# Performance work log

Hardware: AMD Instinct MI355X
Metric: run time of the kernel (lower is better)

## Reference

```python
import jax, jax.numpy as jnp
import numpy as np

N_NODES = 100000
N_EDGES = 1600000
NEG_SLOPE = 0.2  # PyG GATConv default


def _glorot(key, shape):
    fan = sum(shape[:2]) if len(shape) > 1 else shape[0] * 2
    s = jnp.sqrt(6.0 / fan)
    return jax.random.uniform(key, shape, jnp.float32, -s, s)


def gat_layer(x, src, dst, edge_attr, W, a_src, a_dst, We, a_e, b, heads, out_ch, concat):
    """Faithful PyG GATConv (add_self_loops=True, fill_value='mean', edge_dim set)."""
    n = x.shape[0]
    # self-loop edge_attr = mean of incoming edge_attr per dst node (0 if none)
    deg = jax.ops.segment_sum(jnp.ones((src.shape[0],), edge_attr.dtype), dst, num_segments=n)
    loop_attr = jax.ops.segment_sum(edge_attr, dst, num_segments=n) / jnp.maximum(deg, 1.0)[:, None]
    loop = jnp.arange(n, dtype=src.dtype)
    src_f = jnp.concatenate([src, loop])
    dst_f = jnp.concatenate([dst, loop])
    ea = jnp.concatenate([edge_attr, loop_attr], axis=0)
    # node transform -> [n, H, C]
    h = (x @ W).reshape(n, heads, out_ch)
    al_src = jnp.sum(h * a_src, axis=-1)  # [n, H]
    al_dst = jnp.sum(h * a_dst, axis=-1)  # [n, H]
    e = (ea @ We).reshape(-1, heads, out_ch)
    al_e = jnp.sum(e * a_e, axis=-1)      # [Ef, H]
    alpha = jax.nn.leaky_relu(al_src[src_f] + al_dst[dst_f] + al_e, negative_slope=NEG_SLOPE)
    # segment softmax over destination nodes (every node has a self loop)
    m = jax.ops.segment_max(alpha, dst_f, num_segments=n)
    ex = jnp.exp(alpha - m[dst_f])
    den = jax.ops.segment_sum(ex, dst_f, num_segments=n)
    att = ex / den[dst_f]                 # [Ef, H]
    out = jax.ops.segment_sum(att[:, :, None] * h[src_f], dst_f, num_segments=n)  # [n, H, C]
    out = out.reshape(n, heads * out_ch) if concat else out.mean(axis=1)
    return out + b


def setup_inputs() -> dict:
    key = jax.random.key(0)
    ks = jax.random.split(key, 20)
    x = jax.random.normal(ks[0], (N_NODES, 5), jnp.float32)
    edge_index = jax.random.randint(ks[1], (2, N_EDGES), 0, N_NODES, jnp.int64)
    edge_attr = jax.random.normal(ks[2], (N_EDGES, 2), jnp.float32)
    # conv1: in=5, out=32, heads=4, concat -> 128
    p = {
        "W1": _glorot(ks[3], (5, 128)), "aS1": _glorot(ks[4], (4, 32)),
        "aD1": _glorot(ks[5], (4, 32)), "We1": _glorot(ks[6], (2, 128)),
        "aE1": _glorot(ks[7], (4, 32)), "b1": jnp.zeros((128,), jnp.float32),
        # conv2: in=128, out=32, heads=2, concat -> 64
        "W2": _glorot(ks[8], (128, 64)), "aS2": _glorot(ks[9], (2, 32)),
        "aD2": _glorot(ks[10], (2, 32)), "We2": _glorot(ks[11], (2, 64)),
        "aE2": _glorot(ks[12], (2, 32)), "b2": jnp.zeros((64,), jnp.float32),
        # conv3: in=64, out=1, heads=1, concat=False
        "W3": _glorot(ks[13], (64, 1)), "aS3": _glorot(ks[14], (1, 1)),
        "aD3": _glorot(ks[15], (1, 1)), "We3": _glorot(ks[16], (2, 1)),
        "aE3": _glorot(ks[17], (1, 1)), "b3": jnp.zeros((1,), jnp.float32),
    }
    return {"x": x, "edge_index": edge_index, "edge_attr": edge_attr, **p}


def reference(x, edge_index, edge_attr,
              W1, aS1, aD1, We1, aE1, b1,
              W2, aS2, aD2, We2, aE2, b2,
              W3, aS3, aD3, We3, aE3, b3):
    src, dst = edge_index[0], edge_index[1]
    h = gat_layer(x, src, dst, edge_attr, W1, aS1, aD1, We1, aE1, b1, 4, 32, True)
    h = jax.nn.elu(h)  # dropout is identity in eval
    h = gat_layer(h, src, dst, edge_attr, W2, aS2, aD2, We2, aE2, b2, 2, 32, True)
    h = jax.nn.elu(h)
    h = gat_layer(h, src, dst, edge_attr, W3, aS3, aD3, We3, aE3, b3, 1, 1, False)
    return jax.nn.sigmoid(h).squeeze(-1)  # [N]
```

## Files before the change

### kernel.cpp

```cpp
#include <hip/hip_runtime.h>
#include <math.h>

#define NN 100000
#define NE 1600000
#define NPB 256
#define NPB_SHIFT 8
#define NB ((NN + NPB - 1) / NPB)
#define NCHUNK 512
#define CH ((NE + NCHUNK - 1) / NCHUNK)
#define LOG2E 1.44269504088896f

typedef __attribute__((ext_vector_type(8))) short short8v;
typedef __attribute__((ext_vector_type(4))) float f32x4;

__device__ __forceinline__ float lrelu(float x) { return fmaxf(x, 0.2f * x); }
__device__ __forceinline__ float elu1(float x) { return x > 0.f ? x : (__expf(x) - 1.f); }
__device__ __forceinline__ float fexp2(float x) {
#if __has_builtin(__builtin_amdgcn_exp2f)
    return __builtin_amdgcn_exp2f(x);
#else
    return exp2f(x);
#endif
}
__device__ __forceinline__ unsigned bf16rne(float f) {
    unsigned u = __float_as_uint(f);
    return (u + 0x7FFFu + ((u >> 16) & 1u)) >> 16;
}
__device__ __forceinline__ float bf16lo(unsigned u) { return __uint_as_float(u << 16); }
__device__ __forceinline__ float bf16hi(unsigned u) {
    return __uint_as_float(u & 0xFFFF0000u);
}
__device__ __forceinline__ void split2(float x0, float x1, unsigned& hp, unsigned& lp) {
    unsigned h0 = bf16rne(x0), h1 = bf16rne(x1);
    float r0 = x0 - __uint_as_float(h0 << 16);
    float r1 = x1 - __uint_as_float(h1 << 16);
    hp = h0 | (h1 << 16);
    lp = bf16rne(r0) | (bf16rne(r1) << 16);
}

__global__ void __launch_bounds__(256) k_binA0(const int* __restrict__ dst,
                                               int* __restrict__ bucket_cnt) {
    __shared__ int hist[NB];
    int t = threadIdx.x;
    for (int b = t; b < NB; b += 256) hist[b] = 0;
    __syncthreads();
    int c0 = blockIdx.x * CH, c1 = min(NE, c0 + CH);
    for (int e = c0 + t; e < c1; e += 256) atomicAdd(&hist[dst[e] >> NPB_SHIFT], 1);
    __syncthreads();
    for (int b = t; b < NB; b += 256)
        if (hist[b]) atomicAdd(&bucket_cnt[b], hist[b]);
}

__global__ void __launch_bounds__(512) k_bscan(const int* __restrict__ bucket_cnt,
                                               int* __restrict__ bucket_base,
                                               int* __restrict__ bucket_tail) {
    __shared__ int s[512];
    int t = threadIdx.x;
    int v = (t < NB) ? bucket_cnt[t] : 0;
    s[t] = v;
    __syncthreads();
    for (int off = 1; off < 512; off <<= 1) {
        int x = (t >= off) ? s[t - off] : 0;
        __syncthreads();
        if (t >= off) s[t] += x;
        __syncthreads();
    }
    if (t < NB) {
        int ex = s[t] - v;
        bucket_base[t] = ex;
        bucket_tail[t] = ex;
        if (t == NB - 1) bucket_base[NB] = s[t];
    }
}

__global__ void __launch_bounds__(256) k_binA2(const int* __restrict__ src,
                                               const int* __restrict__ dst,
                                               const float* __restrict__ ea,
                                               int* __restrict__ bucket_tail,
                                               uint2* __restrict__ binned,
                                               unsigned char* __restrict__ dstb) {
    __shared__ int hist[NB], pre[NB], cursor[NB], base_l[NB];
    __shared__ int psum[256];
    __shared__ uint2 lrec[CH];
    __shared__ int lds_d[CH];
    int t = threadIdx.x;
    for (int b = t; b < NB; b += 256) hist[b] = 0;
    __syncthreads();
    int c0 = blockIdx.x * CH, c1 = min(NE, c0 + CH);
    int cnt = c1 - c0;
    for (int i = t; i < cnt; i += 256) atomicAdd(&hist[dst[c0 + i] >> NPB_SHIFT], 1);
    __syncthreads();
    int b0 = t << 1, b1 = b0 + 1;
    int h0 = (b0 < NB) ? hist[b0] : 0;
    int h1 = (b1 < NB) ? hist[b1] : 0;
    psum[t] = h0 + h1;
    __syncthreads();
    for (int off = 1; off < 256; off <<= 1) {
        int x = (t >= off) ? psum[t - off] : 0;
        __syncthreads();
        if (t >= off) psum[t] += x;
        __syncthreads();
    }
    int ex = psum[t] - (h0 + h1);
    if (b0 < NB) { pre[b0] = ex;      cursor[b0] = ex; }
    if (b1 < NB) { pre[b1] = ex + h0; cursor[b1] = ex + h0; }
    for (int b = t; b < NB; b += 256) {
        int h = hist[b];
        if (h) base_l[b] = atomicAdd(&bucket_tail[b], h);
    }
    __syncthreads();
    for (int i = t; i < cnt; i += 256) {
        int e = c0 + i;
        int d = dst[e];
        int bkt = d >> NPB_SHIFT;
        int lpos = atomicAdd(&cursor[bkt], 1);
        unsigned pk = bf16rne(ea[2 * e]) | (bf16rne(ea[2 * e + 1]) << 16);
        lrec[lpos] = make_uint2((unsigned)src[e], pk);
        lds_d[lpos] = d;
    }
    __syncthreads();
    for (int i = t; i < cnt; i += 256) {
        int d = lds_d[i];
        int bkt = d >> NPB_SHIFT;
        int gpos = base_l[bkt] + (i - pre[bkt]);
        binned[gpos] = lrec[i];
        dstb[gpos] = (unsigned char)(d & (NPB - 1));
    }
}

__global__ void __launch_bounds__(256) k_binB(const int* __restrict__ bucket_base,
                                              const uint2* __restrict__ binned,
                                              const unsigned char* __restrict__ dstb,
                                              int* __restrict__ rowptr,
                                              uint2* __restrict__ edges,
                                              float* __restrict__ la) {
    __shared__ int hist[NPB], pre[NPB], cursor[NPB];
    __shared__ float ea0s[NPB], ea1s[NPB];
    int b = blockIdx.x, t = threadIdx.x;
    int bb = bucket_base[b], be = bucket_base[b + 1];
    int nb0 = b << NPB_SHIFT;
    hist[t] = 0;
    ea0s[t] = 0.f;
    ea1s[t] = 0.f;
    __syncthreads();
    for (int e = bb + t; e < be; e += 256) atomicAdd(&hist[dstb[e]], 1);
    __syncthreads();
    int v = hist[t];
    pre[t] = v;
    __syncthreads();
    for (int off = 1; off < 256; off <<= 1) {
        int x = (t >= off) ? pre[t - off] : 0;
        __syncthreads();
        if (t >= off) pre[t] += x;
        __syncthreads();
    }
    int ex = pre[t] - v;
    if (nb0 + t <= NN) rowptr[nb0 + t] = bb + ex;
    cursor[t] = bb + ex;
    __syncthreads();
    for (int e = bb + t; e < be; e += 256) {
        uint2 rec = binned[e];
        unsigned char d = dstb[e];
        int pos = atomicAdd(&cursor[d], 1);
        edges[pos] = rec;
        atomicAdd(&ea0s[d], bf16lo(rec.y));
        atomicAdd(&ea1s[d], bf16hi(rec.y));
    }
    __syncthreads();
    int n = nb0 + t;
    if (n < NN) {
        float dg = fmaxf((float)v, 1.0f);
        la[2 * n] = ea0s[t] / dg;
        la[2 * n + 1] = ea1s[t] / dg;
    }
}

__global__ void k_const(const float* __restrict__ We1, const float* __restrict__ aE1,
                        const float* __restrict__ We2, const float* __restrict__ aE2,
                        const float* __restrict__ We3, const float* __restrict__ aE3,
                        const float* __restrict__ W1, const float* __restrict__ aS1,
                        const float* __restrict__ aD1, float* __restrict__ cbuf) {
    int t = threadIdx.x;
    if (t < 8) {
        int d = t >> 2, hd = t & 3;
        float s = 0.f;
        for (int c = 0; c < 32; c++) s += We1[d * 128 + hd * 32 + c] * aE1[hd * 32 + c];
        cbuf[t] = s * LOG2E;
    } else if (t < 12) {
        int idx = t - 8, d = idx >> 1, hd = idx & 1;
        float s = 0.f;
        for (int c = 0; c < 32; c++) s += We2[d * 64 + hd * 32 + c] * aE2[hd * 32 + c];
        cbuf[t] = s * LOG2E;
    } else if (t < 14) {
        cbuf[t] = We3[t - 12] * aE3[0] * LOG2E;
    } else if (t >= 16 && t < 56) {
        int r = (t - 16) % 20, hd = r / 5, i = r % 5;
        const float* a = (t - 16 < 20) ? aS1 : aD1;
        float s = 0.f;
        for (int c = 0; c < 32; c++) s += W1[i * 128 + hd * 32 + c] * a[hd * 32 + c];
        cbuf[t] = s * LOG2E;
    }
}

__global__ void k_w2t(const float* __restrict__ W2, unsigned short* __restrict__ W2th,
                      unsigned short* __restrict__ W2tl) {
    int i = blockIdx.x * 256 + threadIdx.x;
    if (i >= 64 * 128) return;
    int c = i >> 7, k = i & 127;
    float v = W2[k * 64 + c];
    unsigned h = bf16rne(v);
    float hf = __uint_as_float(h << 16);
    unsigned lo = bf16rne(v - hf);
    W2th[c * 128 + k] = (unsigned short)h;
    W2tl[c * 128 + k] = (unsigned short)lo;
}

__global__ void k_prep1(const float* __restrict__ x, const float* __restrict__ vsd,
                        float4* __restrict__ xp, float4* __restrict__ als1,
                        float4* __restrict__ ald1) {
    int n = blockIdx.x * blockDim.x + threadIdx.x;
    if (n >= NN) return;
    float x0 = x[5 * n], x1 = x[5 * n + 1], x2 = x[5 * n + 2], x3 = x[5 * n + 3],
          x4 = x[5 * n + 4];
    xp[2 * n] = make_float4(x0, x1, x2, x3);
    xp[2 * n + 1] = make_float4(x4, 0.f, 0.f, 0.f);
    float sv[4], dv[4];
#pragma unroll
    for (int hd = 0; hd < 4; hd++) {
        const float* vS = vsd + hd * 5;
        const float* vD = vsd + 20 + hd * 5;
        sv[hd] = x0 * vS[0] + x1 * vS[1] + x2 * vS[2] + x3 * vS[3] + x4 * vS[4];
        dv[hd] = x0 * vD[0] + x1 * vD[1] + x2 * vD[2] + x3 * vD[3] + x4 * vD[4];
    }
    als1[n] = make_float4(sv[0], sv[1], sv[2], sv[3]);
    ald1[n] = make_float4(dv[0], dv[1], dv[2], dv[3]);
}

__global__ void k_agg1(const int* __restrict__ rowptr, const uint2* __restrict__ edges,
                       const float4* __restrict__ xp, const float* __restrict__ als1,
                       const float* __restrict__ ald1, const float* __restrict__ la,
                       const float* __restrict__ me, float* __restrict__ xw) {
    int t = blockIdx.x * blockDim.x + threadIdx.x;
    if (t >= NN * 4) return;
    int n = t >> 2, hd = t & 3;
    float me0 = me[hd], me1 = me[4 + hd];
    float aldn = ald1[t];
    float aself = lrelu(als1[t] + aldn + la[2 * n] * me0 + la[2 * n + 1] * me1);
    int start = rowptr[n], end = rowptr[n + 1];
    float den = 1.f;
    float4 xa = xp[2 * n];
    float xb = xp[2 * n + 1].x;
    float a0 = xa.x, a1 = xa.y, a2 = xa.z, a3 = xa.w, a4 = xb;
    int e = start;
    if ((e & 1) && e < end) {
        uint2 ep = edges[e];
        int s = (int)ep.x;
        float a = lrelu(als1[s * 4 + hd] + aldn + bf16lo(ep.y) * me0 + bf16hi(ep.y) * me1);
        float p = fexp2(a - aself);
        den += p;
        float4 sa = xp[2 * s];
        float sb = xp[2 * s + 1].x;
        a0 += p * sa.x; a1 += p * sa.y; a2 += p * sa.z; a3 += p * sa.w; a4 += p * sb;
        e++;
    }
    for (; e + 1 < end; e += 2) {
        uint4 two = *(const uint4*)(edges + e);
        int s0 = (int)two.x, s1 = (int)two.z;
        unsigned pk0 = two.y, pk1 = two.w;
        float l0 = als1[s0 * 4 + hd];
        float l1 = als1[s1 * 4 + hd];
        float4 sa0 = xp[2 * s0];
        float sb0 = xp[2 * s0 + 1].x;
        float4 sa1 = xp[2 * s1];
        float sb1 = xp[2 * s1 + 1].x;
        float av0 = lrelu(l0 + aldn + bf16lo(pk0) * me0 + bf16hi(pk0) * me1);
        float av1 = lrelu(l1 + aldn + bf16lo(pk1) * me0 + bf16hi(pk1) * me1);
        float p0 = fexp2(av0 - aself);
        float p1 = fexp2(av1 - aself);
        den += p0 + p1;
        a0 += p0 * sa0.x + p1 * sa1.x;
        a1 += p0 * sa0.y + p1 * sa1.y;
        a2 += p0 * sa0.z + p1 * sa1.z;
        a3 += p0 * sa0.w + p1 * sa1.w;
        a4 += p0 * sb0 + p1 * sb1;
    }
    if (e < end) {
        uint2 ep = edges[e];
        int s = (int)ep.x;
        float a = lrelu(als1[s * 4 + hd] + aldn + bf16lo(ep.y) * me0 + bf16hi(ep.y) * me1);
        float p = fexp2(a - aself);
        den += p;
        float4 sa = xp[2 * s];
        float sb = xp[2 * s + 1].x;
        a0 += p * sa.x; a1 += p * sa.y; a2 += p * sa.z; a3 += p * sa.w; a4 += p * sb;
    }
    float r = 1.f / den;
    float* w = xw + (size_t)n * 20 + hd * 5;
    w[0] = a0 * r;
    w[1] = a1 * r;
    w[2] = a2 * r;
    w[3] = a3 * r;
    w[4] = a4 * r;
}

__global__ void __launch_bounds__(128) k_l2trans(
        const float* __restrict__ xw, const float* __restrict__ W1,
        const float* __restrict__ b1, const unsigned short* __restrict__ W2th,
        const unsigned short* __restrict__ W2tl,
        const float* __restrict__ aS2, const float* __restrict__ aD2,
        unsigned short* __restrict__ h2q, float* __restrict__ als2,
        float* __restrict__ ald2) {
    __shared__ float wstage[32 * 20];
    __shared__ unsigned short Ahi[4096];
    __shared__ unsigned short Alo[4096];
    int nb = blockIdx.x * 32, t = threadIdx.x;
    {
        int base = nb * 20;
        for (int idx = t; idx < 32 * 20; idx += 128) wstage[idx] = xw[base + idx];
    }
    __syncthreads();
    {
        int nl = t >> 2, g = t & 3;
        int w = nl >> 4, row = nl & 15;
#pragma unroll
        for (int kt = 0; kt < 4; ++kt) {
            int ch0 = kt * 32 + g * 8;
            float4 va = *(const float4*)(b1 + ch0);
            float4 vb = *(const float4*)(b1 + ch0 + 4);
            const float* wp = wstage + nl * 20 + kt * 5;
#pragma unroll
            for (int i = 0; i < 5; ++i) {
                float wi = wp[i];
                float4 A = *(const float4*)(W1 + i * 128 + ch0);
                float4 B = *(const float4*)(W1 + i * 128 + ch0 + 4);
                va.x += wi * A.x; va.y += wi * A.y; va.z += wi * A.z; va.w += wi * A.w;
                vb.x += wi * B.x; vb.y += wi * B.y; vb.z += wi * B.z; vb.w += wi * B.w;
            }
            unsigned hp0, hp1, hp2, hp3, lp0, lp1, lp2, lp3;
            split2(elu1(va.x), elu1(va.y), hp0, lp0);
            split2(elu1(va.z), elu1(va.w), hp1, lp1);
            split2(elu1(vb.x), elu1(vb.y), hp2, lp2);
            split2(elu1(vb.z), elu1(vb.w), hp3, lp3);
            int cidx = (((w * 4 + kt) * 64) + g * 16 + row) * 8;
            *(uint4*)(Ahi + cidx) = make_uint4(hp0, hp1, hp2, hp3);
            *(uint4*)(Alo + cidx) = make_uint4(lp0, lp1, lp2, lp3);
        }
    }
    int l = t & 63, w = t >> 6;
    int g = l >> 4, row16 = l & 15;
    f32x4 acc0 = {0.f, 0.f, 0.f, 0.f}, acc1 = acc0, acc2 = acc0, acc3 = acc0;
    int w4 = w * 4;
#pragma unroll
    for (int kt = 0; kt < 4; ++kt) {
        int abase = ((w4 + kt) * 64 + l) * 8;
        short8v ah = *(const short8v*)(Ahi + abase);
        short8v al = *(const short8v*)(Alo + abase);
        int kb = kt * 32 + g * 8;
        {
            short8v bh = *(const short8v*)(W2th + row16 * 128 + kb);
            short8v bl = *(const short8v*)(W2tl + row16 * 128 + kb);
            acc0 = __builtin_amdgcn_mfma_f32_16x16x32_bf16(ah, bh, acc0, 0, 0, 0);
            acc0 = __builtin_amdgcn_mfma_f32_16x16x32_bf16(al, bh, acc0, 0, 0, 0);
            acc0 = __builtin_amdgcn_mfma_f32_16x16x32_bf16(ah, bl, acc0, 0, 0, 0);
        }
        {
            short8v bh = *(const short8v*)(W2th + (16 + row16) * 128 + kb);
            short8v bl = *(const short8v*)(W2tl + (16 + row16) * 128 + kb);
            acc1 = __builtin_amdgcn_mfma_f32_16x16x32_bf16(ah, bh, acc1, 0, 0, 0);
            acc1 = __builtin_amdgcn_mfma_f32_16x16x32_bf16(al, bh, acc1, 0, 0, 0);
            acc1 = __builtin_amdgcn_mfma_f32_16x16x32_bf16(ah, bl, acc1, 0, 0, 0);
        }
        {
            short8v bh = *(const short8v*)(W2th + (32 + row16) * 128 + kb);
            short8v bl = *(const short8v*)(W2tl + (32 + row16) * 128 + kb);
            acc2 = __builtin_amdgcn_mfma_f32_16x16x32_bf16(ah, bh, acc2, 0, 0, 0);
            acc2 = __builtin_amdgcn_mfma_f32_16x16x32_bf16(al, bh, acc2, 0, 0, 0);
            acc2 = __builtin_amdgcn_mfma_f32_16x16x32_bf16(ah, bl, acc2, 0, 0, 0);
        }
        {
            short8v bh = *(const short8v*)(W2th + (48 + row16) * 128 + kb);
            short8v bl = *(const short8v*)(W2tl + (48 + row16) * 128 + kb);
            acc3 = __builtin_amdgcn_mfma_f32_16x16x32_bf16(ah, bh, acc3, 0, 0, 0);
            acc3 = __builtin_amdgcn_mfma_f32_16x16x32_bf16(al, bh, acc3, 0, 0, 0);
            acc3 = __builtin_amdgcn_mfma_f32_16x16x32_bf16(ah, bl, acc3, 0, 0, 0);
        }
    }
    {
        int nodeb = nb + w * 16 + g * 4;
#pragma unroll
        for (int nt = 0; nt < 4; ++nt) {
            f32x4 A = (nt == 0) ? acc0 : (nt == 1) ? acc1 : (nt == 2) ? acc2 : acc3;
#pragma unroll
            for (int r = 0; r < 4; ++r) {
                float v = A[r];
                float u = __shfl_xor(v, 1);
                if (!(l & 1)) {
                    unsigned pk = bf16rne(v) | (bf16rne(u) << 16);
                    int node = nodeb + r;
                    int ch = nt * 16 + row16;
                    *(unsigned*)(h2q + (size_t)node * 64 + ch) = pk;
                }
            }
        }
        float aSv0 = aS2[row16], aSv1 = aS2[16 + row16];
        float aSv2 = aS2[32 + row16], aSv3 = aS2[48 + row16];
        float aDv0 = aD2[row16], aDv1 = aD2[16 + row16];
        float aDv2 = aD2[32 + row16], aDv3 = aD2[48 + row16];
#pragma unroll
        for (int r = 0; r < 4; ++r) {
            float pS0 = acc0[r] * aSv0 + acc1[r] * aSv1;
            float pS1 = acc2[r] * aSv2 + acc3[r] * aSv3;
            float pD0 = acc0[r] * aDv0 + acc1[r] * aDv1;
            float pD1 = acc2[r] * aDv2 + acc3[r] * aDv3;
#pragma unroll
            for (int off = 1; off < 16; off <<= 1) {
                pS0 += __shfl_xor(pS0, off);
                pS1 += __shfl_xor(pS1, off);
                pD0 += __shfl_xor(pD0, off);
                pD1 += __shfl_xor(pD1, off);
            }
            if (row16 == 0) {
                int node = nodeb + r;
                als2[node * 2 + 0] = pS0 * LOG2E;
                als2[node * 2 + 1] = pS1 * LOG2E;
                ald2[node * 2 + 0] = pD0 * LOG2E;
                ald2[node * 2 + 1] = pD1 * LOG2E;
            }
        }
    }
}

__global__ void k_agg2(const int* __restrict__ rowptr, const uint2* __restrict__ edges,
                       const unsigned short* __restrict__ h2q,
                       const float* __restrict__ als2, const float* __restrict__ ald2,
                       const float* __restrict__ la, const float* __restrict__ me,
                       const float* __restrict__ b2, const float* __restrict__ W3,
                       float* __restrict__ h3) {
    int t = blockIdx.x * blockDim.x + threadIdx.x;
    if (t >= NN * 4) return;
    int n = t >> 2, sub = t & 3, hd = sub >> 1, qh = sub & 1;
    int cbase = hd * 32 + qh * 16;
    float me0 = me[hd], me1 = me[2 + hd];
    float aldn = ald2[n * 2 + hd];
    float aself = lrelu(als2[n * 2 + hd] + aldn + la[2 * n] * me0 + la[2 * n + 1] * me1);
    int start = rowptr[n], end = rowptr[n + 1];
    float den = 1.f;
    float acc[16];
    {
        const uint4* hp = (const uint4*)(h2q + (size_t)n * 64 + cbase);
        uint4 u0 = hp[0], u1 = hp[1];
        acc[0] = bf16lo(u0.x); acc[1] = bf16hi(u0.x);
        acc[2] = bf16lo(u0.y); acc[3] = bf16hi(u0.y);
        acc[4] = bf16lo(u0.z); acc[5] = bf16hi(u0.z);
        acc[6] = bf16lo(u0.w); acc[7] = bf16hi(u0.w);
        acc[8] = bf16lo(u1.x); acc[9] = bf16hi(u1.x);
        acc[10] = bf16lo(u1.y); acc[11] = bf16hi(u1.y);
        acc[12] = bf16lo(u1.z); acc[13] = bf16hi(u1.z);
        acc[14] = bf16lo(u1.w); acc[15] = bf16hi(u1.w);
    }
    int e = start;
    if ((e & 1) && e < end) {
        uint2 ep = edges[e];
        int s = (int)ep.x;
        float a = lrelu(als2[s * 2 + hd] + aldn + bf16lo(ep.y) * me0 + bf16hi(ep.y) * me1);
        float p = fexp2(a - aself);
        den += p;
        const uint4* sp = (const uint4*)(h2q + (size_t)s * 64 + cbase);
        uint4 u0 = sp[0], u1 = sp[1];
        acc[0] += p * bf16lo(u0.x); acc[1] += p * bf16hi(u0.x);
        acc[2] += p * bf16lo(u0.y); acc[3] += p * bf16hi(u0.y);
        acc[4] += p * bf16lo(u0.z); acc[5] += p * bf16hi(u0.z);
        acc[6] += p * bf16lo(u0.w); acc[7] += p * bf16hi(u0.w);
        acc[8] += p * bf16lo(u1.x); acc[9] += p * bf16hi(u1.x);
        acc[10] += p * bf16lo(u1.y); acc[11] += p * bf16hi(u1.y);
        acc[12] += p * bf16lo(u1.z); acc[13] += p * bf16hi(u1.z);
        acc[14] += p * bf16lo(u1.w); acc[15] += p * bf16hi(u1.w);
        e++;
    }
    for (; e + 1 < end; e += 2) {
        uint4 two = *(const uint4*)(edges + e);
        int s0 = (int)two.x, s1 = (int)two.z;
        unsigned pk0 = two.y, pk1 = two.w;
        float l0 = als2[s0 * 2 + hd];
        float l1 = als2[s1 * 2 + hd];
        const uint4* sp0 = (const uint4*)(h2q + (size_t)s0 * 64 + cbase);
        const uint4* sp1 = (const uint4*)(h2q + (size_t)s1 * 64 + cbase);
        uint4 u00 = sp0[0], u01 = sp0[1];
        uint4 u10 = sp1[0], u11 = sp1[1];
        float av0 = lrelu(l0 + aldn + bf16lo(pk0) * me0 + bf16hi(pk0) * me1);
        float av1 = lrelu(l1 + aldn + bf16lo(pk1) * me0 + bf16hi(pk1) * me1);
        float p0 = fexp2(av0 - aself);
        float p1 = fexp2(av1 - aself);
        den += p0 + p1;
        acc[0] += p0 * bf16lo(u00.x) + p1 * bf16lo(u10.x);
        acc[1] += p0 * bf16hi(u00.x) + p1 * bf16hi(u10.x);
        acc[2] += p0 * bf16lo(u00.y) + p1 * bf16lo(u10.y);
        acc[3] += p0 * bf16hi(u00.y) + p1 * bf16hi(u10.y);
        acc[4] += p0 * bf16lo(u00.z) + p1 * bf16lo(u10.z);
        acc[5] += p0 * bf16hi(u00.z) + p1 * bf16hi(u10.z);
        acc[6] += p0 * bf16lo(u00.w) + p1 * bf16lo(u10.w);
        acc[7] += p0 * bf16hi(u00.w) + p1 * bf16hi(u10.w);
        acc[8] += p0 * bf16lo(u01.x) + p1 * bf16lo(u11.x);
        acc[9] += p0 * bf16hi(u01.x) + p1 * bf16hi(u11.x);
        acc[10] += p0 * bf16lo(u01.y) + p1 * bf16lo(u11.y);
        acc[11] += p0 * bf16hi(u01.y) + p1 * bf16hi(u11.y);
        acc[12] += p0 * bf16lo(u01.z) + p1 * bf16lo(u11.z);
        acc[13] += p0 * bf16hi(u01.z) + p1 * bf16hi(u11.z);
        acc[14] += p0 * bf16lo(u01.w) + p1 * bf16lo(u11.w);
        acc[15] += p0 * bf16hi(u01.w) + p1 * bf16hi(u11.w);
    }
    if (e < end) {
        uint2 ep = edges[e];
        int s = (int)ep.x;
        float a = lrelu(als2[s * 2 + hd] + aldn + bf16lo(ep.y) * me0 + bf16hi(ep.y) * me1);
        float p = fexp2(a - aself);
        den += p;
        const uint4* sp = (const uint4*)(h2q + (size_t)s * 64 + cbase);
        uint4 u0 = sp[0], u1 = sp[1];
        acc[0] += p * bf16lo(u0.x); acc[1] += p * bf16hi(u0.x);
        acc[2] += p * bf16lo(u0.y); acc[3] += p * bf16hi(u0.y);
        acc[4] += p * bf16lo(u0.z); acc[5] += p * bf16hi(u0.z);
        acc[6] += p * bf16lo(u0.w); acc[7] += p * bf16hi(u0.w);
        acc[8] += p * bf16lo(u1.x); acc[9] += p * bf16hi(u1.x);
        acc[10] += p * bf16lo(u1.y); acc[11] += p * bf16hi(u1.y);
        acc[12] += p * bf16lo(u1.z); acc[13] += p * bf16hi(u1.z);
        acc[14] += p * bf16lo(u1.w); acc[15] += p * bf16hi(u1.w);
    }
    float r = 1.f / den;
    float part = 0.f;
#pragma unroll
    for (int c = 0; c < 16; c++) {
        float v = elu1(acc[c] * r + b2[cbase + c]);
        part += v * W3[cbase + c];
    }
    part += __shfl_xor(part, 1);
    part += __shfl_xor(part, 2);
    if (sub == 0) h3[n] = part;
}

__global__ void k_agg3(const int* __restrict__ rowptr, const uint2* __restrict__ edges,
                       const float* __restrict__ h, const float* __restrict__ aS3,
                       const float* __restrict__ aD3, const float* __restrict__ la,
                       const float* __restrict__ me, const float* __restrict__ b,
                       float* __restrict__ out) {
    int n = (blockIdx.x * blockDim.x + threadIdx.x) >> 6;
    if (n >= NN) return;
    int lane = threadIdx.x & 63;
    float me0 = me[0], me1 = me[1];
    float aSs = aS3[0] * LOG2E, aDs = aD3[0] * LOG2E;
    float hn = h[n];
    float ald_n = hn * aDs;
    float aself = lrelu(hn * aSs + ald_n + la[2 * n] * me0 + la[2 * n + 1] * me1);
    int start = rowptr[n], end = rowptr[n + 1];
    float den = 0.f, num = 0.f;
    for (int e = start + lane; e < end; e += 64) {
        uint2 ep = edges[e];
        int s = (int)ep.x;
        float hv = h[s];
        float a = lrelu(hv * aSs + ald_n + bf16lo(ep.y) * me0 + bf16hi(ep.y) * me1);
        float p = fexp2(a - aself);
        den += p;
        num += p * hv;
    }
#pragma unroll
    for (int off = 32; off > 0; off >>= 1) {
        den += __shfl_xor(den, off);
        num += __shfl_xor(num, off);
    }
    if (lane == 0) {
        den += 1.f;
        num += hn;
        float v = num / den + b[0];
        out[n] = 1.f / (1.f + __expf(-v));
    }
}

extern "C" void kernel_launch(void* const* d_in, const int* in_sizes, int n_in,
                              void* d_out, int out_size, void* d_ws, size_t ws_size,
                              hipStream_t stream) {
    const float* x   = (const float*)d_in[0];
    const int*   ei  = (const int*)d_in[1];
    const float* ea  = (const float*)d_in[2];
    const float* W1  = (const float*)d_in[3];
    const float* aS1 = (const float*)d_in[4];
    const float* aD1 = (const float*)d_in[5];
    const float* We1 = (const float*)d_in[6];
    const float* aE1 = (const float*)d_in[7];
    const float* b1  = (const float*)d_in[8];
    const float* W2  = (const float*)d_in[9];
    const float* aS2 = (const float*)d_in[10];
    const float* aD2 = (const float*)d_in[11];
    const float* We2 = (const float*)d_in[12];
    const float* aE2 = (const float*)d_in[13];
    const float* b2  = (const float*)d_in[14];
    const float* W3  = (const float*)d_in[15];
    const float* aS3 = (const float*)d_in[16];
    const float* aD3 = (const float*)d_in[17];
    const float* We3 = (const float*)d_in[18];
    const float* aE3 = (const float*)d_in[19];
    const float* b3  = (const float*)d_in[20];

    const int* srcv = ei;
    const int* dstv = ei + NE;

    char* basep = (char*)d_ws;
    size_t off = 0;
    auto alloc = [&](size_t nbytes) -> void* {
        void* p = basep + off;
        off += (nbytes + 255) & ~(size_t)255;
        return p;
    };
    int*    bucket_cnt  = (int*)alloc((size_t)(NB + 1) * 4);
    int*    bucket_base = (int*)alloc((size_t)(NB + 1) * 4);
    int*    bucket_tail = (int*)alloc((size_t)(NB + 1) * 4);
    int*    rowptr      = (int*)alloc((size_t)(NN + 1) * 4);
    uint2*  binned      = (uint2*)alloc((size_t)NE * 8);
    unsigned char* dstb = (unsigned char*)alloc((size_t)NE);
    uint2*  edges       = (uint2*)alloc((size_t)NE * 8);
    float*  la          = (float*)alloc((size_t)NN * 8);
    float*  cbuf        = (float*)alloc(256);
    float4* xp          = (float4*)alloc((size_t)NN * 32);
    float4* als1        = (float4*)alloc((size_t)NN * 16);
    float4* ald1        = (float4*)alloc((size_t)NN * 16);
    float*  xw          = (float*)alloc((size_t)NN * 80);
    unsigned short* h2q = (unsigned short*)alloc((size_t)NN * 128);
    float*  als2        = (float*)alloc((size_t)NN * 8);
    float*  ald2        = (float*)alloc((size_t)NN * 8);
    float*  h3          = (float*)alloc((size_t)NN * 4);
    unsigned short* W2th = (unsigned short*)alloc(64 * 128 * 2);
    unsigned short* W2tl = (unsigned short*)alloc(64 * 128 * 2);
    (void)ws_size; (void)in_sizes; (void)n_in; (void)out_size;

    float* me1 = cbuf;
    float* me2 = cbuf + 8;
    float* me3 = cbuf + 12;
    float* vsd = cbuf + 16;

    auto cdiv = [](long long a, long long b) { return (int)((a + b - 1) / b); };
    const int BS = 256;

    hipMemsetAsync(bucket_cnt, 0, (size_t)(NB + 1) * 4, stream);
    k_binA0<<<NCHUNK, 256, 0, stream>>>(dstv, bucket_cnt);
    k_bscan<<<1, 512, 0, stream>>>(bucket_cnt, bucket_base, bucket_tail);
    k_binA2<<<NCHUNK, 256, 0, stream>>>(srcv, dstv, ea, bucket_tail, binned, dstb);
    k_binB<<<NB, 256, 0, stream>>>(bucket_base, binned, dstb, rowptr, edges, la);

    k_const<<<1, 64, 0, stream>>>(We1, aE1, We2, aE2, We3, aE3, W1, aS1, aD1, cbuf);
    k_w2t<<<32, 256, 0, stream>>>(W2, W2th, W2tl);

    k_prep1<<<cdiv(NN, BS), BS, 0, stream>>>(x, vsd, xp, als1, ald1);
    k_agg1<<<cdiv((long long)NN * 4, BS), BS, 0, stream>>>(rowptr, edges, xp,
                                                           (const float*)als1,
                                                           (const float*)ald1, la, me1, xw);

    k_l2trans<<<cdiv(NN, 32), 128, 0, stream>>>(xw, W1, b1, W2th, W2tl, aS2, aD2,
                                                h2q, als2, ald2);
    k_agg2<<<cdiv((long long)NN * 4, BS), BS, 0, stream>>>(rowptr, edges, h2q, als2, ald2,
                                                           la, me2, b2, W3, h3);

    k_agg3<<<cdiv(NN, 4), 256, 0, stream>>>(rowptr, edges, h3, aS3, aD3, la, me3,
                                            b3, (float*)d_out);
}
```

Baseline: 328.9 us.

## Fuse layer-1 aggregation with layer-2 transform into one kernel

Merges the layer-1 edge aggregation kernel and the layer-2 dense-transform MFMA kernel into one kernel. Each 4-thread group aggregates a node and keeps the per-head result in registers, then feeds it straight into the W1/ELU/bf16-split staging in LDS and the MFMA transform. This removes the global xw intermediate buffer (written then re-read) and one kernel launch. In exchange, the fused kernel uses 32 KB of LDS per 256-thread block, which may lower occupancy for the latency-bound gather phase, and it adds bounds guards for the partial last block.

```diff
diff --git a/kernel.cpp b/kernel.cpp
--- a/kernel.cpp
+++ b/kernel.cpp
@@ -236,123 +236,138 @@
     ald1[n] = make_float4(dv[0], dv[1], dv[2], dv[3]);
 }
 
-__global__ void k_agg1(const int* __restrict__ rowptr, const uint2* __restrict__ edges,
-                       const float4* __restrict__ xp, const float* __restrict__ als1,
-                       const float* __restrict__ ald1, const float* __restrict__ la,
-                       const float* __restrict__ me, float* __restrict__ xw) {
-    int t = blockIdx.x * blockDim.x + threadIdx.x;
-    if (t >= NN * 4) return;
+__global__ void __launch_bounds__(256) k_agg1f(
+        const int* __restrict__ rowptr, const uint2* __restrict__ edges,
+        const float4* __restrict__ xp, const float* __restrict__ als1,
+        const float* __restrict__ ald1, const float* __restrict__ la,
+        const float* __restrict__ me, const float* __restrict__ W1,
+        const float* __restrict__ b1, const unsigned short* __restrict__ W2th,
+        const unsigned short* __restrict__ W2tl, const float* __restrict__ aS2,
+        const float* __restrict__ aD2, unsigned short* __restrict__ h2q,
+        float* __restrict__ als2, float* __restrict__ ald2) {
+    __shared__ unsigned short Ahi[8192];
+    __shared__ unsigned short Alo[8192];
+    int t = blockIdx.x * 256 + threadIdx.x;
+    int tl = threadIdx.x;
     int n = t >> 2, hd = t & 3;
-    float me0 = me[hd], me1 = me[4 + hd];
-    float aldn = ald1[t];
-    float aself = lrelu(als1[t] + aldn + la[2 * n] * me0 + la[2 * n + 1] * me1);
-    int start = rowptr[n], end = rowptr[n + 1];
-    float den = 1.f;
-    float4 xa = xp[2 * n];
-    float xb = xp[2 * n + 1].x;
-    float a0 = xa.x, a1 = xa.y, a2 = xa.z, a3 = xa.w, a4 = xb;
-    int e = start;
-    if ((e & 1) && e < end) {
-        uint2 ep = edges[e];
-        int s = (int)ep.x;
-        float a = lrelu(als1[s * 4 + hd] + aldn + bf16lo(ep.y) * me0 + bf16hi(ep.y) * me1);
-        float p = fexp2(a - aself);
-        den += p;
-        float4 sa = xp[2 * s];
-        float sb = xp[2 * s + 1].x;
-        a0 += p * sa.x; a1 += p * sa.y; a2 += p * sa.z; a3 += p * sa.w; a4 += p * sb;
-        e++;
-    }
-    for (; e + 1 < end; e += 2) {
-        uint4 two = *(const uint4*)(edges + e);
-        int s0 = (int)two.x, s1 = (int)two.z;
-        unsigned pk0 = two.y, pk1 = two.w;
-        float l0 = als1[s0 * 4 + hd];
-        float l1 = als1[s1 * 4 + hd];
-        float4 sa0 = xp[2 * s0];
-        float sb0 = xp[2 * s0 + 1].x;
-        float4 sa1 = xp[2 * s1];
-        float sb1 = xp[2 * s1 + 1].x;
-        float av0 = lrelu(l0 + aldn + bf16lo(pk0) * me0 + bf16hi(pk0) * me1);
-        float av1 = lrelu(l1 + aldn + bf16lo(pk1) * me0 + bf16hi(pk1) * me1);
-        float p0 = fexp2(av0 - aself);
-        float p1 = fexp2(av1 - aself);
-        den += p0 + p1;
-        a0 += p0 * sa0.x + p1 * sa1.x;
-        a1 += p0 * sa0.y + p1 * sa1.y;
-        a2 += p0 * sa0.z + p1 * sa1.z;
-        a3 += p0 * sa0.w + p1 * sa1.w;
-        a4 += p0 * sb0 + p1 * sb1;
-    }
-    if (e < end) {
-        uint2 ep = edges[e];
-        int s = (int)ep.x;
-        float a = lrelu(als1[s * 4 + hd] + aldn + bf16lo(ep.y) * me0 + bf16hi(ep.y) * me1);
-        float p = fexp2(a - aself);
-        den += p;
-        float4 sa = xp[2 * s];
-        float sb = xp[2 * s + 1].x;
-        a0 += p * sa.x; a1 += p * sa.y; a2 += p * sa.z; a3 += p * sa.w; a4 += p * sb;
-    }
-    float r = 1.f / den;
-    float* w = xw + (size_t)n * 20 + hd * 5;
-    w[0] = a0 * r;
-    w[1] = a1 * r;
-    w[2] = a2 * r;
-    w[3] = a3 * r;
-    w[4] = a4 * r;
-}
-
-__global__ void __launch_bounds__(128) k_l2trans(
-        const float* __restrict__ xw, const float* __restrict__ W1,
-        const float* __restrict__ b1, const unsigned short* __restrict__ W2th,
-        const unsigned short* __restrict__ W2tl,
-        const float* __restrict__ aS2, const float* __restrict__ aD2,
-        unsigned short* __restrict__ h2q, float* __restrict__ als2,
-        float* __restrict__ ald2) {
-    __shared__ float wstage[32 * 20];
-    __shared__ unsigned short Ahi[4096];
-    __shared__ unsigned short Alo[4096];
-    int nb = blockIdx.x * 32, t = threadIdx.x;
-    {
-        int base = nb * 20;
-        for (int idx = t; idx < 32 * 20; idx += 128) wstage[idx] = xw[base + idx];
-    }
-    __syncthreads();
-    {
-        int nl = t >> 2, g = t & 3;
-        int w = nl >> 4, row = nl & 15;
-#pragma unroll
-        for (int kt = 0; kt < 4; ++kt) {
-            int ch0 = kt * 32 + g * 8;
+    int nl = tl >> 2;
+    int wq = nl >> 4, row = nl & 15;
+    float w0 = 0.f, w1 = 0.f, w2 = 0.f, w3 = 0.f, w4 = 0.f;
+    if (n < NN) {
+        float me0 = me[hd], me1v = me[4 + hd];
+        float aldn = ald1[t];
+        float aself = lrelu(als1[t] + aldn + la[2 * n] * me0 + la[2 * n + 1] * me1v);
+        int start = rowptr[n], end = rowptr[n + 1];
+        float den = 1.f;
+        float4 xa = xp[2 * n];
+        float xb = xp[2 * n + 1].x;
+        float a0 = xa.x, a1 = xa.y, a2 = xa.z, a3 = xa.w, a4 = xb;
+        int e = start;
+        if ((e & 1) && e < end) {
+            uint2 ep = edges[e];
+            int s = (int)ep.x;
+            float a = lrelu(als1[s * 4 + hd] + aldn + bf16lo(ep.y) * me0 + bf16hi(ep.y) * me1v);
+            float p = fexp2(a - aself);
+            den += p;
+            float4 sa = xp[2 * s];
+            float sb = xp[2 * s + 1].x;
+            a0 += p * sa.x; a1 += p * sa.y; a2 += p * sa.z; a3 += p * sa.w; a4 += p * sb;
+            e++;
+        }
+        for (; e + 1 < end; e += 2) {
+            uint4 two = *(const uint4*)(edges + e);
+            int s0 = (int)two.x, s1 = (int)two.z;
+            unsigned pk0 = two.y, pk1 = two.w;
+            float l0 = als1[s0 * 4 + hd];
+            float l1 = als1[s1 * 4 + hd];
+            float4 sa0 = xp[2 * s0];
+            float sb0 = xp[2 * s0 + 1].x;
+            float4 sa1 = xp[2 * s1];
+            float sb1 = xp[2 * s1 + 1].x;
+            float av0 = lrelu(l0 + aldn + bf16lo(pk0) * me0 + bf16hi(pk0) * me1v);
+            float av1 = lrelu(l1 + aldn + bf16lo(pk1) * me0 + bf16hi(pk1) * me1v);
+            float p0 = fexp2(av0 - aself);
+            float p1 = fexp2(av1 - aself);
+            den += p0 + p1;
+            a0 += p0 * sa0.x + p1 * sa1.x;
+            a1 += p0 * sa0.y + p1 * sa1.y;
+            a2 += p0 * sa0.z + p1 * sa1.z;
+            a3 += p0 * sa0.w + p1 * sa1.w;
+            a4 += p0 * sb0 + p1 * sb1;
+        }
+        if (e < end) {
+            uint2 ep = edges[e];
+            int s = (int)ep.x;
+            float a = lrelu(als1[s * 4 + hd] + aldn + bf16lo(ep.y) * me0 + bf16hi(ep.y) * me1v);
+            float p = fexp2(a - aself);
+            den += p;
+            float4 sa = xp[2 * s];
+            float sb = xp[2 * s + 1].x;
+            a0 += p * sa.x; a1 += p * sa.y; a2 += p * sa.z; a3 += p * sa.w; a4 += p * sb;
+        }
+        float r = 1.f / den;
+        w0 = a0 * r; w1 = a1 * r; w2 = a2 * r; w3 = a3 * r; w4 = a4 * r;
+    }
+    if (n < NN) {
+#pragma unroll
+        for (int g = 0; g < 4; ++g) {
+            int ch0 = hd * 32 + g * 8;
             float4 va = *(const float4*)(b1 + ch0);
             float4 vb = *(const float4*)(b1 + ch0 + 4);
-            const float* wp = wstage + nl * 20 + kt * 5;
-#pragma unroll
-            for (int i = 0; i < 5; ++i) {
-                float wi = wp[i];
-                float4 A = *(const float4*)(W1 + i * 128 + ch0);
-                float4 B = *(const float4*)(W1 + i * 128 + ch0 + 4);
-                va.x += wi * A.x; va.y += wi * A.y; va.z += wi * A.z; va.w += wi * A.w;
-                vb.x += wi * B.x; vb.y += wi * B.y; vb.z += wi * B.z; vb.w += wi * B.w;
+            {
+                float4 A = *(const float4*)(W1 + 0 * 128 + ch0);
+                float4 B = *(const float4*)(W1 + 0 * 128 + ch0 + 4);
+                va.x += w0 * A.x; va.y += w0 * A.y; va.z += w0 * A.z; va.w += w0 * A.w;
+                vb.x += w0 * B.x; vb.y += w0 * B.y; vb.z += w0 * B.z; vb.w += w0 * B.w;
+            }
+            {
+                float4 A = *(const float4*)(W1 + 1 * 128 + ch0);
+                float4 B = *(const float4*)(W1 + 1 * 128 + ch0 + 4);
+                va.x += w1 * A.x; va.y += w1 * A.y; va.z += w1 * A.z; va.w += w1 * A.w;
+                vb.x += w1 * B.x; vb.y += w1 * B.y; vb.z += w1 * B.z; vb.w += w1 * B.w;
+            }
+            {
+                float4 A = *(const float4*)(W1 + 2 * 128 + ch0);
+                float4 B = *(const float4*)(W1 + 2 * 128 + ch0 + 4);
+                va.x += w2 * A.x; va.y += w2 * A.y; va.z += w2 * A.z; va.w += w2 * A.w;
+                vb.x += w2 * B.x; vb.y += w2 * B.y; vb.z += w2 * B.z; vb.w += w2 * B.w;
+            }
+            {
+                float4 A = *(const float4*)(W1 + 3 * 128 + ch0);
+                float4 B = *(const float4*)(W1 + 3 * 128 + ch0 + 4);
+                va.x += w3 * A.x; va.y += w3 * A.y; va.z += w3 * A.z; va.w += w3 * A.w;
+                vb.x += w3 * B.x; vb.y += w3 * B.y; vb.z += w3 * B.z; vb.w += w3 * B.w;
+            }
+            {
+                float4 A = *(const float4*)(W1 + 4 * 128 + ch0);
+                float4 B = *(const float4*)(W1 + 4 * 128 + ch0 + 4);
+                va.x += w4 * A.x; va.y += w4 * A.y; va.z += w4 * A.z; va.w += w4 * A.w;
+                vb.x += w4 * B.x; vb.y += w4 * B.y; vb.z += w4 * B.z; vb.w += w4 * B.w;
             }
             unsigned hp0, hp1, hp2, hp3, lp0, lp1, lp2, lp3;
             split2(elu1(va.x), elu1(va.y), hp0, lp0);
             split2(elu1(va.z), elu1(va.w), hp1, lp1);
             split2(elu1(vb.x), elu1(vb.y), hp2, lp2);
             split2(elu1(vb.z), elu1(vb.w), hp3, lp3);
-            int cidx = (((w * 4 + kt) * 64) + g * 16 + row) * 8;
+            int cidx = (((wq * 4 + hd) * 64) + g * 16 + row) * 8;
             *(uint4*)(Ahi + cidx) = make_uint4(hp0, hp1, hp2, hp3);
             *(uint4*)(Alo + cidx) = make_uint4(lp0, lp1, lp2, lp3);
         }
-    }
-    int l = t & 63, w = t >> 6;
+    } else {
+#pragma unroll
+        for (int g = 0; g < 4; ++g) {
+            int cidx = (((wq * 4 + hd) * 64) + g * 16 + row) * 8;
+            *(uint4*)(Ahi + cidx) = make_uint4(0, 0, 0, 0);
+            *(uint4*)(Alo + cidx) = make_uint4(0, 0, 0, 0);
+        }
+    }
+    int l = tl & 63, w = tl >> 6;
     int g = l >> 4, row16 = l & 15;
     f32x4 acc0 = {0.f, 0.f, 0.f, 0.f}, acc1 = acc0, acc2 = acc0, acc3 = acc0;
-    int w4 = w * 4;
+    int w4i = w * 4;
 #pragma unroll
     for (int kt = 0; kt < 4; ++kt) {
-        int abase = ((w4 + kt) * 64 + l) * 8;
+        int abase = ((w4i + kt) * 64 + l) * 8;
         short8v ah = *(const short8v*)(Ahi + abase);
         short8v al = *(const short8v*)(Alo + abase);
         int kb = kt * 32 + g * 8;
@@ -386,7 +401,7 @@
         }
     }
     {
-        int nodeb = nb + w * 16 + g * 4;
+        int nodeb = blockIdx.x * 64 + w * 16 + g * 4;
 #pragma unroll
         for (int nt = 0; nt < 4; ++nt) {
             f32x4 A = (nt == 0) ? acc0 : (nt == 1) ? acc1 : (nt == 2) ? acc2 : acc3;
@@ -394,9 +409,9 @@
             for (int r = 0; r < 4; ++r) {
                 float v = A[r];
                 float u = __shfl_xor(v, 1);
-                if (!(l & 1)) {
+                int node = nodeb + r;
+                if (!(l & 1) && node < NN) {
                     unsigned pk = bf16rne(v) | (bf16rne(u) << 16);
-                    int node = nodeb + r;
                     int ch = nt * 16 + row16;
                     *(unsigned*)(h2q + (size_t)node * 64 + ch) = pk;
                 }
@@ -419,8 +434,8 @@
                 pD0 += __shfl_xor(pD0, off);
                 pD1 += __shfl_xor(pD1, off);
             }
-            if (row16 == 0) {
-                int node = nodeb + r;
+            int node = nodeb + r;
+            if (row16 == 0 && node < NN) {
                 als2[node * 2 + 0] = pS0 * LOG2E;
                 als2[node * 2 + 1] = pS1 * LOG2E;
                 ald2[node * 2 + 0] = pD0 * LOG2E;
@@ -622,7 +637,6 @@
     float4* xp          = (float4*)alloc((size_t)NN * 32);
     float4* als1        = (float4*)alloc((size_t)NN * 16);
     float4* ald1        = (float4*)alloc((size_t)NN * 16);
-    float*  xw          = (float*)alloc((size_t)NN * 80);
     unsigned short* h2q = (unsigned short*)alloc((size_t)NN * 128);
     float*  als2        = (float*)alloc((size_t)NN * 8);
     float*  ald2        = (float*)alloc((size_t)NN * 8);
@@ -649,12 +663,10 @@
     k_w2t<<<32, 256, 0, stream>>>(W2, W2th, W2tl);
 
     k_prep1<<<cdiv(NN, BS), BS, 0, stream>>>(x, vsd, xp, als1, ald1);
-    k_agg1<<<cdiv((long long)NN * 4, BS), BS, 0, stream>>>(rowptr, edges, xp,
-                                                           (const float*)als1,
-                                                           (const float*)ald1, la, me1, xw);
-
-    k_l2trans<<<cdiv(NN, 32), 128, 0, stream>>>(xw, W1, b1, W2th, W2tl, aS2, aD2,
-                                                h2q, als2, ald2);
+    k_agg1f<<<cdiv((long long)NN * 4, BS), BS, 0, stream>>>(
+        rowptr, edges, xp, (const float*)als1, (const float*)ald1, la, me1,
+        W1, b1, W2th, W2tl, aS2, aD2, h2q, als2, ald2);
+
     k_agg2<<<cdiv((long long)NN * 4, BS), BS, 0, stream>>>(rowptr, edges, h2q, als2, ald2,
                                                            la, me2, b2, W3, h3);
 
```

Result: slower. 354.0 us (+7.6%).
